# Optimization experiments

Hardware: AMD Instinct MI355X
Metric: run time of the kernel (lower is better)

The kernel has to match this reference:

```python
import jax, jax.numpy as jnp
import numpy as np

IMG = 512
LEVELS = (2, 3, 4, 5, 6)
SIZES = (16.0, 32.0, 64.0, 128.0, 256.0)
SCALES = tuple(2.0 ** (i / 3.0) for i in range(3))
ASPECTS = (0.5, 1.0, 2.0)
PRE_NMS = 1000
POST_NMS = 1000
IOU_T = 0.7
SCORE_T = 0.0
CROP = 7
NUM_CLASSES = 80

PARAMS = ('w_l2','b_l2','w_l3','b_l3','w_l4','b_l4','w_l5','b_l5','w_l6','b_l6',
          'w_o2','b_o2','w_o3','b_o3','w_o4','b_o4','w_o5','b_o5','w_o6','b_o6',
          'w_rpn','b_rpn','w_obj','b_obj','w_dlt','b_dlt',
          'w_fc1','b_fc1','w_fc2','b_fc2','w_box','b_box','w_cls','b_cls')

def conv(x, w, b, relu=False):
    y = jax.lax.conv_general_dilated(x, w, (1, 1), 'SAME', dimension_numbers=('NHWC', 'HWIO', 'NHWC')) + b
    return jax.nn.relu(y) if relu else y

def upsample2(x):
    return jnp.repeat(jnp.repeat(x, 2, axis=1), 2, axis=2)

def maxpool2(x):
    return jax.lax.reduce_window(x, -jnp.inf, jax.lax.max, (1, 2, 2, 1), (1, 2, 2, 1), 'VALID')

def make_anchors():
    # keras_cv AnchorGenerator: yxyx, 3 scales x 3 aspect ratios per location, clipped to image
    levels = []
    for lvl, size in zip(LEVELS, SIZES):
        stride = 2 ** lvl
        fs = IMG // stride
        ctr = (np.arange(fs) + 0.5) * stride
        hw = np.array([[size * sc / np.sqrt(ar), size * sc * np.sqrt(ar)] for sc in SCALES for ar in ASPECTS])
        cyx = np.stack(np.meshgrid(ctr, ctr, indexing='ij'), -1)  # [fs,fs,2]
        a = np.concatenate([cyx[:, :, None, :] - hw / 2.0, cyx[:, :, None, :] + hw / 2.0], -1).reshape(-1, 4)
        levels.append(np.clip(a, 0.0, IMG))
    return jnp.asarray(np.concatenate(levels, 0), jnp.float32)  # [196416,4]

def fpn(c2, c3, c4, c5, p):
    c6 = maxpool2(c5)
    p6 = conv(c6, p['w_l6'], p['b_l6'])
    p5 = conv(c5, p['w_l5'], p['b_l5']) + upsample2(p6)
    p4 = conv(c4, p['w_l4'], p['b_l4']) + upsample2(p5)
    p3 = conv(c3, p['w_l3'], p['b_l3']) + upsample2(p4)
    p2 = conv(c2, p['w_l2'], p['b_l2']) + upsample2(p3)
    return [conv(x, p['w_o%d' % l], p['b_o%d' % l]) for x, l in zip((p2, p3, p4, p5, p6), LEVELS)]

def rpn(fmaps, p):
    boxes, scores = [], []
    for f in fmaps:
        t = conv(f, p['w_rpn'], p['b_rpn'], relu=True)
        s = conv(t, p['w_obj'], p['b_obj'])
        d = conv(t, p['w_dlt'], p['b_dlt'])
        B = f.shape[0]
        boxes.append(d.reshape(B, -1, 4))
        scores.append(s.reshape(B, -1))
    return jnp.concatenate(boxes, 1), jnp.concatenate(scores, 1)

def decode(anchors, deltas):
    # _decode_deltas_to_boxes (no variance) then center_yxhw -> yxyx
    ahw = anchors[:, 2:] - anchors[:, :2]
    act = anchors[:, :2] + ahw * 0.5
    cyx = deltas[..., :2] * ahw + act
    hw = jnp.exp(deltas[..., 2:]) * ahw
    return jnp.concatenate([cyx - hw * 0.5, cyx + hw * 0.5], -1)

def nms_single(boxes, scores):
    # greedy NMS on top PRE_NMS proposals, padded to POST_NMS outputs
    sc, order = jax.lax.top_k(scores, PRE_NMS)
    b = boxes[order]
    y1, x1, y2, x2 = b[:, 0], b[:, 1], b[:, 2], b[:, 3]
    area = (y2 - y1) * (x2 - x1)

    def body(i, keep):
        iy1 = jnp.maximum(y1[i], y1)
        ix1 = jnp.maximum(x1[i], x1)
        iy2 = jnp.minimum(y2[i], y2)
        ix2 = jnp.minimum(x2[i], x2)
        inter = jnp.maximum(iy2 - iy1, 0.0) * jnp.maximum(ix2 - ix1, 0.0)
        iou = inter / (area[i] + area - inter + 1e-8)
        suppress = (iou > IOU_T) & (jnp.arange(PRE_NMS) > i) & keep[i]
        return keep & (~suppress)

    keep = jax.lax.fori_loop(0, PRE_NMS, body, sc > SCORE_T)
    idx = jnp.cumsum(keep) - 1
    slot = jnp.where(keep & (idx < POST_NMS), idx, POST_NMS)
    return jnp.zeros((POST_NMS, 4), boxes.dtype).at[slot].set(b, mode='drop')

def pad_stack(fmaps):
    Hm = fmaps[0].shape[1]
    return jnp.stack([jnp.pad(f, ((0, 0), (0, Hm - f.shape[1]), (0, Hm - f.shape[2]), (0, 0))) for f in fmaps], 1)

def roi_align(feats, rois):
    # multilevel crop-and-resize: 14x14 bilinear samples (offset 0.5) -> 2x2 avg pool -> 7x7
    S = CROP * 2

    def one(feat, box):
        h = box[2] - box[0]
        w = box[3] - box[1]
        size = jnp.sqrt(jnp.maximum(h * w, 1e-8))
        lvl = jnp.clip(jnp.floor(jnp.log2(size / 224.0) + 4.0), 2, 6).astype(jnp.int32)
        stride_i = jnp.left_shift(1, lvl)
        stride = stride_i.astype(jnp.float32)
        fs_i = IMG // stride_i
        fs = fs_i.astype(jnp.float32)
        yy = jnp.clip(box[0] / stride + (jnp.arange(S) + 0.5) * (h / stride) / S - 0.5, 0.0, fs - 1.0)
        xx = jnp.clip(box[1] / stride + (jnp.arange(S) + 0.5) * (w / stride) / S - 0.5, 0.0, fs - 1.0)
        y0 = jnp.floor(yy).astype(jnp.int32)
        x0 = jnp.floor(xx).astype(jnp.int32)
        y1 = jnp.minimum(y0 + 1, fs_i - 1)
        x1 = jnp.minimum(x0 + 1, fs_i - 1)
        wy = (yy - y0)[:, None, None]
        wx = (xx - x0)[None, :, None]
        fm = feat[lvl - 2]
        v00 = fm[y0[:, None], x0[None, :]]
        v01 = fm[y0[:, None], x1[None, :]]
        v10 = fm[y1[:, None], x0[None, :]]
        v11 = fm[y1[:, None], x1[None, :]]
        val = (1.0 - wy) * ((1.0 - wx) * v00 + wx * v01) + wy * ((1.0 - wx) * v10 + wx * v11)
        return val.reshape(CROP, 2, CROP, 2, val.shape[-1]).mean(axis=(1, 3))

    return jax.vmap(lambda f, r: jax.vmap(lambda b: one(f, b))(r))(feats, rois)

def forward(c2, c3, c4, c5, p):
    fmaps = fpn(c2, c3, c4, c5, p)
    rpn_boxes, rpn_scores = rpn(fmaps, p)
    anchors = make_anchors()
    decoded = decode(anchors, rpn_boxes)
    rois = jax.lax.stop_gradient(jax.vmap(nms_single)(decoded, rpn_scores))  # [B,1000,4]
    feats = roi_align(pad_stack(fmaps), rois)  # [B,1000,7,7,256]
    B, R = feats.shape[0], feats.shape[1]
    x = feats.reshape(B, R, -1)
    x = jax.nn.relu(x @ p['w_fc1'] + p['b_fc1'])
    x = jax.nn.relu(x @ p['w_fc2'] + p['b_fc2'])
    return rois, x @ p['w_box'] + p['b_box'], x @ p['w_cls'] + p['b_cls']

def setup_inputs() -> dict:
    key = jax.random.key(0)
    ks = iter(jax.random.split(key, 64))
    def rnd(shape, s=1.0):
        return jax.random.normal(next(ks), shape, jnp.float32) * s
    B = 2
    inp = {
        'c2': rnd((B, 128, 128, 256)), 'c3': rnd((B, 64, 64, 512)),
        'c4': rnd((B, 32, 32, 1024)), 'c5': rnd((B, 16, 16, 2048)),
    }
    lat_in = {2: 256, 3: 512, 4: 1024, 5: 2048, 6: 2048}
    for l in LEVELS:
        inp['w_l%d' % l] = rnd((1, 1, lat_in[l], 256), 0.02)
        inp['b_l%d' % l] = jnp.zeros((256,), jnp.float32)
        inp['w_o%d' % l] = rnd((3, 3, 256, 256), 0.02)
        inp['b_o%d' % l] = jnp.zeros((256,), jnp.float32)
    inp['w_rpn'] = rnd((3, 3, 256, 256), 0.02); inp['b_rpn'] = jnp.zeros((256,), jnp.float32)
    inp['w_obj'] = rnd((1, 1, 256, 9), 0.02); inp['b_obj'] = jnp.zeros((9,), jnp.float32)
    inp['w_dlt'] = rnd((1, 1, 256, 36), 0.02); inp['b_dlt'] = jnp.zeros((36,), jnp.float32)
    F = CROP * CROP * 256
    inp['w_fc1'] = rnd((F, 1024), 0.01); inp['b_fc1'] = jnp.zeros((1024,), jnp.float32)
    inp['w_fc2'] = rnd((1024, 1024), 0.02); inp['b_fc2'] = jnp.zeros((1024,), jnp.float32)
    inp['w_box'] = rnd((1024, 4), 0.02); inp['b_box'] = jnp.zeros((4,), jnp.float32)
    inp['w_cls'] = rnd((1024, NUM_CLASSES + 1), 0.02); inp['b_cls'] = jnp.zeros((NUM_CLASSES + 1,), jnp.float32)
    return inp

def reference(c2, c3, c4, c5, w_l2, b_l2, w_l3, b_l3, w_l4, b_l4, w_l5, b_l5, w_l6, b_l6,
              w_o2, b_o2, w_o3, b_o3, w_o4, b_o4, w_o5, b_o5, w_o6, b_o6,
              w_rpn, b_rpn, w_obj, b_obj, w_dlt, b_dlt,
              w_fc1, b_fc1, w_fc2, b_fc2, w_box, b_box, w_cls, b_cls):
    loc = locals()
    p = {k: loc[k] for k in PARAMS}
    return forward(c2, c3, c4, c5, p)
```

## Files before the change

### kernel.cpp

```cpp
#include <hip/hip_runtime.h>
#include <math.h>


#define NUM_ANCH 196416

typedef double d4 __attribute__((ext_vector_type(4)));
typedef __attribute__((ext_vector_type(8))) short bf8_t;
typedef __attribute__((ext_vector_type(4))) float f4_t;
typedef _Float16 h8_t __attribute__((ext_vector_type(8)));

__device__ inline unsigned short f2bf(float x) {
  unsigned u = __float_as_uint(x);
  unsigned r = (u + 0x7fffu + ((u >> 16) & 1u)) >> 16;
  return (unsigned short)r;
}
__device__ inline float bf2f(unsigned short h) {
  return __uint_as_float(((unsigned)h) << 16);
}

__global__ void maxpool_kernel(const float* __restrict__ in, float* __restrict__ out) {
  int idx = blockIdx.x * 256 + threadIdx.x;
  int c = idx & 2047;
  int x = (idx >> 11) & 7;
  int y = (idx >> 14) & 7;
  int b = idx >> 17;
  const float* p = in + (((size_t)b * 16 + 2 * y) * 16 + 2 * x) * 2048 + c;
  float m = fmaxf(fmaxf(p[0], p[2048]), fmaxf(p[16 * 2048], p[16 * 2048 + 2048]));
  out[idx] = m;
}

template <int CIN>
__global__ __launch_bounds__(256) void lateral_d(
    const float* __restrict__ in, const float* __restrict__ w,
    const float* __restrict__ bias, double* __restrict__ out) {
  const int t = threadIdx.x;
  const size_t pix0 = (size_t)blockIdx.x * 4;
  double b = (double)bias[t];
  double a0 = b, a1 = b, a2 = b, a3 = b;
  const float* i0 = in + pix0 * CIN;
  for (int ci = 0; ci < CIN; ++ci) {
    double wv = (double)w[ci * 256 + t];
    a0 += (double)i0[ci] * wv;
    a1 += (double)i0[CIN + ci] * wv;
    a2 += (double)i0[2 * CIN + ci] * wv;
    a3 += (double)i0[3 * CIN + ci] * wv;
  }
  out[(pix0 + 0) * 256 + t] = a0;
  out[(pix0 + 1) * 256 + t] = a1;
  out[(pix0 + 2) * 256 + t] = a2;
  out[(pix0 + 3) * 256 + t] = a3;
}

__global__ void upadd_d(double* __restrict__ fine, const double* __restrict__ coarse,
                        int Hf, int Wf) {
  int idx = blockIdx.x * 256 + threadIdx.x;
  int c = idx & 255;
  int rem = idx >> 8;
  int x = rem % Wf; rem /= Wf;
  int y = rem % Hf;
  int b = rem / Hf;
  fine[idx] += coarse[(((size_t)b * (Hf >> 1) + (y >> 1)) * (Wf >> 1) + (x >> 1)) * 256 + c];
}

__global__ __launch_bounds__(256) void wsplit_f16(
    const float* __restrict__ W, unsigned short* __restrict__ PH,
    unsigned short* __restrict__ PL) {
  int id = blockIdx.x * 256 + threadIdx.x;
  int co = id & 255, ci = (id >> 8) & 255, p9 = id >> 16;
  float w = W[id];
  _Float16 wh = (_Float16)w;
  float rw = (w - (float)wh) * 4096.0f;
  _Float16 wl = (_Float16)rw;
  int q = (p9 * 8 + (ci >> 5)) * 16 + (co >> 4);
  int idx = q * 512 + (co & 15) * 32 + (ci & 31);
  PH[idx] = __builtin_bit_cast(unsigned short, wh);
  PL[idx] = __builtin_bit_cast(unsigned short, wl);
}

struct ConvArgsU {
  const double* inD[5];
  const unsigned short* inH[5];
  const unsigned short* inL[5];
  float* outF[5];
  unsigned short* outH[5];
  unsigned short* outL[5];
  double* outD[5];
  const unsigned short* wH[5];
  const unsigned short* wL[5];
  const float* bias[5];
  int H[5];
  int nbx[5];
  int off[6];
};

template <bool PLANES, bool RELU, bool OSPLIT>
__global__ __launch_bounds__(512, 4) void conv3x3_u(ConvArgsU A) {
  __shared__ uint4 smemq[34816 / 16];
  char* sh = (char*)smemq;
  const int bx = blockIdx.x;
  int l = 0;
#pragma unroll
  for (int i = 1; i < 5; ++i)
    if (bx >= A.off[i]) l = i;
  const int rel = bx - A.off[l];
  const int H = A.H[l];
  const int W = H;
  const int nbx = A.nbx[l];
  const int x0 = (rel % nbx) * 32;
  const int y = (rel / nbx) % H;
  const int b = rel / (nbx * H);
  const unsigned short* __restrict__ wHp = A.wH[l];
  const unsigned short* __restrict__ wLp = A.wL[l];
  const float* __restrict__ bias = A.bias[l];

  const int t = threadIdx.x;
  const int lane = t & 63;
  const int wq = t >> 6;
  const int lm = lane & 15;
  const int lq = lane >> 4;

  d4 dacc[2][2];
#pragma unroll
  for (int mt = 0; mt < 2; ++mt)
#pragma unroll
    for (int nt = 0; nt < 2; ++nt) {
      double bv = (double)bias[wq * 32 + nt * 16 + lm];
      dacc[mt][nt] = (d4){bv, bv, bv, bv};
    }

  const int cst = (t & 127) * 2;
  const int prow = t >> 7;
  const int c16 = (t & 31) * 8;
  const int pp0 = t >> 5;

  for (int ky = 0; ky < 3; ++ky) {
    const int gy = y + ky - 1;
    const bool rowok = (gy >= 0 && gy < H);
    __syncthreads();
    if (PLANES) {
      const unsigned short* __restrict__ inH = A.inH[l];
      const unsigned short* __restrict__ inL = A.inL[l];
      for (int pp = pp0; pp < 34; pp += 16) {
        int gx = x0 + pp - 1;
        uint4 vh = {0u, 0u, 0u, 0u}, vl = {0u, 0u, 0u, 0u};
        if (rowok && gx >= 0 && gx < W) {
          size_t base = (((size_t)b * H + gy) * W + gx) * 256 + c16;
          vh = *(const uint4*)&inH[base];
          vl = *(const uint4*)&inL[base];
        }
        int bo = pp * 512 + ((c16 * 2) ^ ((pp & 7) << 4));
        *(uint4*)(sh + bo) = vh;
        *(uint4*)(sh + 17408 + bo) = vl;
      }
    } else {
      const double* __restrict__ inD = A.inD[l];
      for (int pp = prow; pp < 34; pp += 4) {
        int gx = x0 + pp - 1;
        double xv0 = 0.0, xv1 = 0.0;
        if (rowok && gx >= 0 && gx < W) {
          const double* ptr = inD + (((size_t)b * H + gy) * W + gx) * 256 + cst;
          xv0 = ptr[0];
          xv1 = ptr[1];
        }
        _Float16 h0 = (_Float16)((float)xv0);
        _Float16 h1 = (_Float16)((float)xv1);
        float r0 = (float)(xv0 - (double)(float)h0) * 4096.0f;
        float r1 = (float)(xv1 - (double)(float)h1) * 4096.0f;
        _Float16 l0 = (_Float16)r0, l1 = (_Float16)r1;
        unsigned hp = (unsigned)__builtin_bit_cast(unsigned short, h0) |
                      ((unsigned)__builtin_bit_cast(unsigned short, h1) << 16);
        unsigned lp = (unsigned)__builtin_bit_cast(unsigned short, l0) |
                      ((unsigned)__builtin_bit_cast(unsigned short, l1) << 16);
        int bo = pp * 512 + ((cst * 2) ^ ((pp & 7) << 4));
        *(unsigned*)(sh + bo) = hp;
        *(unsigned*)(sh + 17408 + bo) = lp;
      }
    }
    __syncthreads();

    f4_t accA[2][2], accB[2][2];
#pragma unroll
    for (int mt = 0; mt < 2; ++mt)
#pragma unroll
      for (int nt = 0; nt < 2; ++nt) {
        accA[mt][nt] = (f4_t){0.f, 0.f, 0.f, 0.f};
        accB[mt][nt] = (f4_t){0.f, 0.f, 0.f, 0.f};
      }

    for (int kx = 0; kx < 3; ++kx) {
      const int P0 = (ky * 3 + kx) * 8;
      for (int kt = 0; kt < 8; ++kt) {
        h8_t aH[2], aL[2];
#pragma unroll
        for (int mt = 0; mt < 2; ++mt) {
          int pix = mt * 16 + lm + kx;
          int bo = pix * 512 + ((kt * 64 + lq * 16) ^ ((pix & 7) << 4));
          aH[mt] = *(const h8_t*)(sh + bo);
          aL[mt] = *(const h8_t*)(sh + 17408 + bo);
        }
#pragma unroll
        for (int nt = 0; nt < 2; ++nt) {
          size_t eo = (size_t)((P0 + kt) * 16 + wq * 2 + nt) * 512 + lm * 32 + lq * 8;
          h8_t bH = *(const h8_t*)(wHp + eo);
          h8_t bL = *(const h8_t*)(wLp + eo);
#pragma unroll
          for (int mt = 0; mt < 2; ++mt) {
            accB[mt][nt] = __builtin_amdgcn_mfma_f32_16x16x32_f16(aH[mt], bL, accB[mt][nt], 0, 0, 0);
            accB[mt][nt] = __builtin_amdgcn_mfma_f32_16x16x32_f16(aL[mt], bH, accB[mt][nt], 0, 0, 0);
            accA[mt][nt] = __builtin_amdgcn_mfma_f32_16x16x32_f16(aH[mt], bH, accA[mt][nt], 0, 0, 0);
          }
        }
      }
    }
#pragma unroll
    for (int mt = 0; mt < 2; ++mt)
#pragma unroll
      for (int nt = 0; nt < 2; ++nt)
#pragma unroll
        for (int r = 0; r < 4; ++r)
          dacc[mt][nt][r] += (double)accA[mt][nt][r] +
                             (double)accB[mt][nt][r] * (1.0 / 4096.0);
  }

#pragma unroll
  for (int mt = 0; mt < 2; ++mt)
#pragma unroll
    for (int nt = 0; nt < 2; ++nt) {
      int cout = wq * 32 + nt * 16 + lm;
#pragma unroll
      for (int r = 0; r < 4; ++r) {
        int gx = x0 + mt * 16 + lq * 4 + r;
        if (gx < W) {
          double v = dacc[mt][nt][r];
          if (RELU) v = fmax(v, 0.0);
          size_t idx = (((size_t)b * H + y) * W + gx) * 256 + cout;
          if (OSPLIT) {
            _Float16 hh = (_Float16)((float)v);
            float rr = (float)(v - (double)(float)hh) * 4096.0f;
            _Float16 ll = (_Float16)rr;
            A.outF[l][idx] = (float)v;
            A.outH[l][idx] = __builtin_bit_cast(unsigned short, hh);
            A.outL[l][idx] = __builtin_bit_cast(unsigned short, ll);
          } else {
            A.outD[l][idx] = v;
          }
        }
      }
    }
}

struct AnchorHW { double hh[9]; double ww[9]; };

__global__ __launch_bounds__(64) void rpn_head_d(
    const double* __restrict__ tmap,
    const float* __restrict__ w_obj, const float* __restrict__ b_obj,
    const float* __restrict__ w_dlt, const float* __restrict__ b_dlt,
    double* __restrict__ scores, double* __restrict__ boxes,
    int H, int W, int a_off, double stride, AnchorHW anc) {
  __shared__ double tv[256];
  __shared__ double dlt[36];
  const int t = threadIdx.x;
  const int x = blockIdx.x, y = blockIdx.y, b = blockIdx.z;
  const double* px = tmap + (((size_t)b * H + y) * W + x) * 256;
  tv[t] = px[t]; tv[t + 64] = px[t + 64]; tv[t + 128] = px[t + 128]; tv[t + 192] = px[t + 192];
  __syncthreads();
  double sacc = 0.0;
  if (t < 9) {
    sacc = (double)b_obj[t];
    for (int ci = 0; ci < 256; ++ci) sacc += tv[ci] * (double)w_obj[ci * 9 + t];
  } else if (t < 45) {
    int j = t - 9;
    double a = (double)b_dlt[j];
    for (int ci = 0; ci < 256; ++ci) a += tv[ci] * (double)w_dlt[ci * 36 + j];
    dlt[j] = a;
  }
  __syncthreads();
  if (t < 9) {
    int ai = a_off + (y * W + x) * 9 + t;
    scores[(size_t)b * NUM_ANCH + ai] = sacc;
    double cy = (y + 0.5) * stride, cx = (x + 0.5) * stride;
    double hh = anc.hh[t], ww = anc.ww[t];
    float ay1 = (float)fmin(fmax(cy - hh * 0.5, 0.0), 512.0);
    float ax1 = (float)fmin(fmax(cx - ww * 0.5, 0.0), 512.0);
    float ay2 = (float)fmin(fmax(cy + hh * 0.5, 0.0), 512.0);
    float ax2 = (float)fmin(fmax(cx + ww * 0.5, 0.0), 512.0);
    float ahf = ay2 - ay1, awf = ax2 - ax1;
    float actyf = ay1 + ahf * 0.5f, actxf = ax1 + awf * 0.5f;
    double dy = dlt[t * 4 + 0], dx = dlt[t * 4 + 1];
    double dh = dlt[t * 4 + 2], dw = dlt[t * 4 + 3];
    double ncy = dy * (double)ahf + (double)actyf;
    double ncx = dx * (double)awf + (double)actxf;
    double nh = exp(dh) * (double)ahf;
    double nw = exp(dw) * (double)awf;
    double* bo = boxes + ((size_t)b * NUM_ANCH + ai) * 4;
    bo[0] = ncy - nh * 0.5;
    bo[1] = ncx - nw * 0.5;
    bo[2] = ncy + nh * 0.5;
    bo[3] = ncx + nw * 0.5;
  }
}

__device__ inline unsigned long long dkey(double f) {
  unsigned long long u = (unsigned long long)__double_as_longlong(f);
  return u ^ ((unsigned long long)((long long)u >> 63) | 0x8000000000000000ull);
}

__global__ __launch_bounds__(1024) void topk_d(
    const double* __restrict__ scores, const double* __restrict__ boxes,
    double* __restrict__ ss, double* __restrict__ sb) {
  const int A = NUM_ANCH;
  __shared__ unsigned hist[256];
  __shared__ unsigned long long kk[2048];
  __shared__ unsigned id[2048];
  __shared__ unsigned long long s_prefix;
  __shared__ unsigned s_need, s_cnt;
  const int b = blockIdx.x, t = threadIdx.x;
  const double* sc = scores + (size_t)b * A;
  if (t == 0) { s_prefix = 0ull; s_need = 1000; s_cnt = 0; }
  __syncthreads();
  for (int r = 0; r < 8; ++r) {
    if (t < 256) hist[t] = 0;
    __syncthreads();
    const int shift = 56 - 8 * r;
    const unsigned long long prefix = s_prefix;
    unsigned long long maskHigh = 0ull;
    if (r != 0) maskHigh = (~0ull) << (shift + 8);
    for (int i = t; i < A; i += 1024) {
      unsigned long long k = dkey(sc[i]);
      if ((k & maskHigh) == prefix) atomicAdd(&hist[(unsigned)(k >> shift) & 255u], 1u);
    }
    __syncthreads();
    if (t == 0) {
      unsigned need = s_need, cum = 0;
      for (int bin = 255; bin >= 0; --bin) {
        cum += hist[bin];
        if (cum >= need) {
          s_prefix = prefix | ((unsigned long long)bin << shift);
          s_need = need - (cum - hist[bin]);
          break;
        }
      }
    }
    __syncthreads();
  }
  const unsigned long long K = s_prefix;
  for (int i = t; i < A; i += 1024) {
    unsigned long long k = dkey(sc[i]);
    if (k >= K) {
      unsigned pos = atomicAdd(&s_cnt, 1u);
      if (pos < 2048) { kk[pos] = k; id[pos] = (unsigned)i; }
    }
  }
  __syncthreads();
  unsigned cnt = s_cnt;
  for (int i = t; i < 2048; i += 1024)
    if (i >= cnt) { kk[i] = 0ull; id[i] = 0xFFFFFFFFu; }
  __syncthreads();
  for (int k = 2; k <= 2048; k <<= 1) {
    for (int j = k >> 1; j > 0; j >>= 1) {
#pragma unroll
      for (int u = 0; u < 2; ++u) {
        int i = t + u * 1024;
        int ixj = i ^ j;
        if (ixj > i) {
          unsigned long long ka = kk[i], kc = kk[ixj];
          unsigned ia = id[i], ic = id[ixj];
          bool cPrec = (kc > ka) || (kc == ka && ic < ia);
          bool up = (i & k) != 0;
          if (cPrec != up) { kk[i] = kc; kk[ixj] = ka; id[i] = ic; id[ixj] = ia; }
        }
      }
      __syncthreads();
    }
  }
  if (t < 1000) {
    unsigned idx = id[t];
    ss[b * 1000 + t] = sc[idx];
    const double* bp = boxes + ((size_t)b * A + idx) * 4;
    double* op = sb + (b * 1000 + t) * 4;
    op[0] = bp[0]; op[1] = bp[1]; op[2] = bp[2]; op[3] = bp[3];
  }
}

__global__ void suppmat_d(const double* __restrict__ sb,
                          unsigned long long* __restrict__ supp) {
  int g = blockIdx.x * 256 + threadIdx.x;
  int w = g & 15;
  int i = (g >> 4) % 1000;
  int b = g / 16000;
  const double* bx = sb + b * 4000;
  double y1 = bx[i * 4 + 0], x1 = bx[i * 4 + 1], y2 = bx[i * 4 + 2], x2 = bx[i * 4 + 3];
  double ai = (y2 - y1) * (x2 - x1);
  unsigned long long m = 0;
  for (int q = 0; q < 64; ++q) {
    int j = w * 64 + q;
    if (j > i && j < 1000) {
      double by1 = bx[j * 4 + 0], bx1 = bx[j * 4 + 1], by2 = bx[j * 4 + 2], bx2 = bx[j * 4 + 3];
      double aj = (by2 - by1) * (bx2 - bx1);
      double iy1 = fmax(y1, by1), ix1 = fmax(x1, bx1);
      double iy2 = fmin(y2, by2), ix2 = fmin(x2, bx2);
      double inter = fmax(iy2 - iy1, 0.0) * fmax(ix2 - ix1, 0.0);
      double iou = inter / (ai + aj - inter + 1e-8);
      if (iou > 0.7) m |= (1ull << q);
    }
  }
  supp[g] = m;
}

__global__ __launch_bounds__(64) void nms_reduce_d(
    const double* __restrict__ ss, const double* __restrict__ sb,
    const unsigned long long* __restrict__ supp,
    float* __restrict__ rois, double* __restrict__ rois64) {
  __shared__ unsigned long long aliveS[16];
  __shared__ int pref[16];
  const int b = blockIdx.x, lane = threadIdx.x;
  unsigned long long myword = 0;
  if (lane < 16) {
    for (int q = 0; q < 64; ++q) {
      int j = lane * 64 + q;
      if (j < 1000 && ss[b * 1000 + j] > 0.0) myword |= (1ull << q);
    }
  }
  const unsigned long long* sp = supp + (size_t)b * 16000;
  unsigned long long cur = (lane < 16) ? sp[lane] : 0ull;
  for (int i = 0; i < 1000; ++i) {
    unsigned long long nxt = (lane < 16 && i < 999) ? sp[(i + 1) * 16 + lane] : 0ull;
    unsigned long long wv = __shfl(myword, i >> 6);
    if ((wv >> (i & 63)) & 1ull) {
      if (lane < 16) myword &= ~cur;
    }
    cur = nxt;
  }
  if (lane < 16) aliveS[lane] = myword;
  __syncthreads();
  if (lane == 0) {
    int s = 0;
    for (int w = 0; w < 16; ++w) { pref[w] = s; s += __popcll(aliveS[w]); }
  }
  float* ro = rois + b * 4000;
  double* rd = rois64 + b * 4000;
  for (int k = lane; k < 4000; k += 64) { ro[k] = 0.0f; rd[k] = 0.0; }
  __syncthreads();
  for (int j = lane; j < 1000; j += 64) {
    int w = j >> 6;
    unsigned long long word = aliveS[w];
    if ((word >> (j & 63)) & 1ull) {
      unsigned long long below = (j & 63) ? (word & ((1ull << (j & 63)) - 1ull)) : 0ull;
      int slot = pref[w] + __popcll(below);
      const double* bp = sb + (b * 1000 + j) * 4;
      ro[slot * 4 + 0] = (float)bp[0]; ro[slot * 4 + 1] = (float)bp[1];
      ro[slot * 4 + 2] = (float)bp[2]; ro[slot * 4 + 3] = (float)bp[3];
      rd[slot * 4 + 0] = bp[0]; rd[slot * 4 + 1] = bp[1];
      rd[slot * 4 + 2] = bp[2]; rd[slot * 4 + 3] = bp[3];
    }
  }
}

__global__ __launch_bounds__(256) void roi_align_d(
    const float* __restrict__ o2, const float* __restrict__ o3,
    const float* __restrict__ o4, const float* __restrict__ o5,
    const float* __restrict__ o6, const double* __restrict__ rois64,
    unsigned short* __restrict__ featsH, unsigned short* __restrict__ featsL) {
  __shared__ double s_wy[14], s_wx[14];
  __shared__ int s_y0[14], s_y1[14], s_x0[14], s_x1[14];
  const int t = threadIdx.x;
  const int b = blockIdx.x / 1000, r = blockIdx.x % 1000;
  const double* box = rois64 + (b * 1000 + r) * 4;
  double b0 = box[0], b1 = box[1], b2 = box[2], b3 = box[3];
  double h = b2 - b0, w = b3 - b1;
  double size = sqrt(fmax(h * w, 1e-8));
  double lf = floor(log2(size / 224.0) + 4.0);
  lf = fmin(fmax(lf, 2.0), 6.0);
  int lvl = (int)lf;
  int stride_i = 1 << lvl;
  double stride = (double)stride_i;
  int fs_i = 512 >> lvl;
  double fs = (double)fs_i;
  if (t < 14) {
    double v = b0 / stride + ((t + 0.5) * (h / stride)) / 14.0 - 0.5;
    v = fmin(fmax(v, 0.0), fs - 1.0);
    int i0 = (int)floor(v);
    s_y0[t] = i0; s_y1[t] = min(i0 + 1, fs_i - 1); s_wy[t] = v - (double)i0;
  } else if (t >= 64 && t < 78) {
    int u = t - 64;
    double v = b1 / stride + ((u + 0.5) * (w / stride)) / 14.0 - 0.5;
    v = fmin(fmax(v, 0.0), fs - 1.0);
    int i0 = (int)floor(v);
    s_x0[u] = i0; s_x1[u] = min(i0 + 1, fs_i - 1); s_wx[u] = v - (double)i0;
  }
  __syncthreads();
  const float* omaps[5] = {o2, o3, o4, o5, o6};
  const float* fm = omaps[lvl - 2] + (size_t)b * fs_i * fs_i * 256 + t;
  size_t obase = ((size_t)(b * 1000 + r) * 49) * 256 + t;
  for (int oy = 0; oy < 7; ++oy) {
    double acc[7] = {0, 0, 0, 0, 0, 0, 0};
#pragma unroll
    for (int sy = 0; sy < 2; ++sy) {
      int yy = oy * 2 + sy;
      int y0 = s_y0[yy], y1 = s_y1[yy];
      double wy = s_wy[yy];
      const float* r0 = fm + (size_t)y0 * fs_i * 256;
      const float* r1 = fm + (size_t)y1 * fs_i * 256;
      for (int ox = 0; ox < 7; ++ox) {
#pragma unroll
        for (int sx = 0; sx < 2; ++sx) {
          int xx = ox * 2 + sx;
          int x0 = s_x0[xx], x1 = s_x1[xx];
          double wx = s_wx[xx];
          double v00 = (double)r0[x0 * 256], v01 = (double)r0[x1 * 256];
          double v10 = (double)r1[x0 * 256], v11 = (double)r1[x1 * 256];
          double val = (1.0 - wy) * ((1.0 - wx) * v00 + wx * v01) +
                       wy * ((1.0 - wx) * v10 + wx * v11);
          acc[ox] += val;
        }
      }
    }
    for (int ox = 0; ox < 7; ++ox) {
      float v = (float)(acc[ox] * 0.25);
      unsigned short hh = f2bf(v);
      size_t idx = obase + (size_t)(oy * 7 + ox) * 256;
      featsH[idx] = hh;
      featsL[idx] = f2bf(v - bf2f(hh));
    }
  }
}

__global__ __launch_bounds__(256) void split_transpose(
    const float* __restrict__ W, unsigned short* __restrict__ TH,
    unsigned short* __restrict__ TL, int K, int N) {
  __shared__ unsigned short shh[32 * 33], shl[32 * 33];
  const int kt = blockIdx.y * 32, nt = blockIdx.x * 32;
  const int tx = threadIdx.x & 31, ty = threadIdx.x >> 5;
  for (int yy = ty; yy < 32; yy += 8) {
    float v = W[(size_t)(kt + yy) * N + nt + tx];
    unsigned short h = f2bf(v);
    shh[yy * 33 + tx] = h;
    shl[yy * 33 + tx] = f2bf(v - bf2f(h));
  }
  __syncthreads();
  for (int yy = ty; yy < 32; yy += 8) {
    TH[(size_t)(nt + yy) * K + kt + tx] = shh[tx * 33 + yy];
    TL[(size_t)(nt + yy) * K + kt + tx] = shl[tx * 33 + yy];
  }
}

struct GemmPArgs {
  const unsigned short* AH;
  const unsigned short* AL;
  const unsigned short* BTH;
  const unsigned short* BTL;
  float* P[4];
  int M, N, K, KC;
};

__global__ __launch_bounds__(256) void gemm_mfma_partial(GemmPArgs G) {
  __shared__ __align__(16) unsigned short AsH[128 * 40], AsL[128 * 40];
  __shared__ __align__(16) unsigned short BsH[128 * 40], BsL[128 * 40];
  const int t = threadIdx.x;
  const int lane = t & 63;
  const int wave = t >> 6;
  const int lm = lane & 15, lq = lane >> 4;
  const int wn = wave & 1, wm = wave >> 1;
  const int m0 = blockIdx.y * 128, n0 = blockIdx.x * 128;
  const int kc = blockIdx.z;
  const int kbeg = kc * G.KC, kend = kbeg + G.KC;
  const int M = G.M, N = G.N, K = G.K;
  float* __restrict__ C = G.P[kc];
  const unsigned short* __restrict__ AH = G.AH;
  const unsigned short* __restrict__ AL = G.AL;
  const unsigned short* __restrict__ BTH = G.BTH;
  const unsigned short* __restrict__ BTL = G.BTL;
  const int sr = t >> 1;
  const int sk = (t & 1) * 16;

  f4_t acc[4][4];
#pragma unroll
  for (int mt = 0; mt < 4; ++mt)
#pragma unroll
    for (int nt = 0; nt < 4; ++nt) acc[mt][nt] = (f4_t){0.f, 0.f, 0.f, 0.f};

  const uint4 zz = {0u, 0u, 0u, 0u};
  for (int k0 = kbeg; k0 < kend; k0 += 32) {
    __syncthreads();
    {
      uint4 vh0 = zz, vh1 = zz, vl0 = zz, vl1 = zz;
      if (m0 + sr < M) {
        size_t off = (size_t)(m0 + sr) * K + k0 + sk;
        vh0 = *(const uint4*)&AH[off];
        vh1 = *(const uint4*)&AH[off + 8];
        vl0 = *(const uint4*)&AL[off];
        vl1 = *(const uint4*)&AL[off + 8];
      }
      *(uint4*)&AsH[sr * 40 + sk] = vh0;
      *(uint4*)&AsH[sr * 40 + sk + 8] = vh1;
      *(uint4*)&AsL[sr * 40 + sk] = vl0;
      *(uint4*)&AsL[sr * 40 + sk + 8] = vl1;
    }
    {
      size_t off = (size_t)(n0 + sr) * K + k0 + sk;
      *(uint4*)&BsH[sr * 40 + sk] = *(const uint4*)&BTH[off];
      *(uint4*)&BsH[sr * 40 + sk + 8] = *(const uint4*)&BTH[off + 8];
      *(uint4*)&BsL[sr * 40 + sk] = *(const uint4*)&BTL[off];
      *(uint4*)&BsL[sr * 40 + sk + 8] = *(const uint4*)&BTL[off + 8];
    }
    __syncthreads();

    bf8_t aH[4], aL[4], bH[4], bL[4];
#pragma unroll
    for (int mt = 0; mt < 4; ++mt) {
      int idx = (wm * 64 + mt * 16 + lm) * 40 + lq * 8;
      aH[mt] = *(const bf8_t*)&AsH[idx];
      aL[mt] = *(const bf8_t*)&AsL[idx];
    }
#pragma unroll
    for (int nt = 0; nt < 4; ++nt) {
      int idx = (wn * 64 + nt * 16 + lm) * 40 + lq * 8;
      bH[nt] = *(const bf8_t*)&BsH[idx];
      bL[nt] = *(const bf8_t*)&BsL[idx];
    }
#pragma unroll
    for (int mt = 0; mt < 4; ++mt)
#pragma unroll
      for (int nt = 0; nt < 4; ++nt) {
        f4_t a0 = acc[mt][nt];
        a0 = __builtin_amdgcn_mfma_f32_16x16x32_bf16(aL[mt], bH[nt], a0, 0, 0, 0);
        a0 = __builtin_amdgcn_mfma_f32_16x16x32_bf16(aH[mt], bL[nt], a0, 0, 0, 0);
        a0 = __builtin_amdgcn_mfma_f32_16x16x32_bf16(aH[mt], bH[nt], a0, 0, 0, 0);
        acc[mt][nt] = a0;
      }
  }
#pragma unroll
  for (int mt = 0; mt < 4; ++mt) {
#pragma unroll
    for (int nt = 0; nt < 4; ++nt) {
      int ncol = n0 + wn * 64 + nt * 16 + lm;
#pragma unroll
      for (int r = 0; r < 4; ++r) {
        int m = m0 + wm * 64 + mt * 16 + lq * 4 + r;
        if (m < M) C[(size_t)m * N + ncol] = acc[mt][nt][r];
      }
    }
  }
}

__global__ void reduce4_split(const float* __restrict__ p0, const float* __restrict__ p1,
                              const float* __restrict__ p2, const float* __restrict__ p3,
                              const float* __restrict__ bias,
                              unsigned short* __restrict__ H, unsigned short* __restrict__ L,
                              int n) {
  int i = blockIdx.x * 256 + threadIdx.x;
  if (i < n) {
    float v = ((p0[i] + p1[i]) + p2[i]) + p3[i] + bias[i & 1023];
    v = fmaxf(v, 0.0f);
    unsigned short h = f2bf(v);
    H[i] = h;
    L[i] = f2bf(v - bf2f(h));
  }
}

__global__ void reduce4_f32(const float* __restrict__ p0, const float* __restrict__ p1,
                            const float* __restrict__ p2, const float* __restrict__ p3,
                            const float* __restrict__ bias, float* __restrict__ C, int n) {
  int i = blockIdx.x * 256 + threadIdx.x;
  if (i < n) {
    float v = ((p0[i] + p1[i]) + p2[i]) + p3[i] + bias[i & 1023];
    C[i] = fmaxf(v, 0.0f);
  }
}

__global__ __launch_bounds__(128) void boxcls_kernel(
    const float* __restrict__ x, const float* __restrict__ w_box,
    const float* __restrict__ b_box, const float* __restrict__ w_cls,
    const float* __restrict__ b_cls, float* __restrict__ out) {
  __shared__ float xv[1024];
  const int t = threadIdx.x;
  const int row = blockIdx.x;
  const float* xp = x + (size_t)row * 1024;
#pragma unroll
  for (int k = 0; k < 8; ++k) xv[k * 128 + t] = xp[k * 128 + t];
  __syncthreads();
  if (t < 4) {
    float acc = b_box[t];
    for (int k = 0; k < 1024; ++k) acc += xv[k] * w_box[k * 4 + t];
    out[8000 + row * 4 + t] = acc;
  } else if (t < 85) {
    int j = t - 4;
    float acc = b_cls[j];
    for (int k = 0; k < 1024; ++k) acc += xv[k] * w_cls[k * 81 + j];
    out[16000 + row * 81 + j] = acc;
  }
}

extern "C" void kernel_launch(void* const* d_in, const int* in_sizes, int n_in,
                              void* d_out, int out_size, void* d_ws, size_t ws_size,
                              hipStream_t stream) {
  (void)in_sizes; (void)n_in; (void)out_size; (void)ws_size;

  const float* c_in[4] = {(const float*)d_in[0], (const float*)d_in[1],
                          (const float*)d_in[2], (const float*)d_in[3]};
  const float *w_l[5], *b_l[5], *w_o[5], *b_o[5];
  for (int l = 0; l < 5; ++l) {
    w_l[l] = (const float*)d_in[4 + l * 4 + 0];
    b_l[l] = (const float*)d_in[4 + l * 4 + 1];
    w_o[l] = (const float*)d_in[4 + l * 4 + 2];
    b_o[l] = (const float*)d_in[4 + l * 4 + 3];
  }
  const float* w_rpn = (const float*)d_in[24];
  const float* b_rpn = (const float*)d_in[25];
  const float* w_obj = (const float*)d_in[26];
  const float* b_obj = (const float*)d_in[27];
  const float* w_dlt = (const float*)d_in[28];
  const float* b_dlt = (const float*)d_in[29];
  const float* w_fc1 = (const float*)d_in[30];
  const float* b_fc1 = (const float*)d_in[31];
  const float* w_fc2 = (const float*)d_in[32];
  const float* b_fc2 = (const float*)d_in[33];
  const float* w_box = (const float*)d_in[34];
  const float* b_box = (const float*)d_in[35];
  const float* w_cls = (const float*)d_in[36];
  const float* b_cls = (const float*)d_in[37];

  char* W8 = (char*)d_ws;
  float* oF32 = (float*)(W8 + 0);
  unsigned short* oH = (unsigned short*)(W8 + 44695552);
  unsigned short* oL = (unsigned short*)(W8 + 67043328);
  double* p64 = (double*)(W8 + 89391104);
  float* c6buf = (float*)(W8 + 178782208);
  double* scores = (double*)(W8 + 179830784);
  double* boxes = (double*)(W8 + 182973440);
  double* ssb = (double*)(W8 + 195544064);
  double* sbb = (double*)(W8 + 195560064);
  double* rois64 = (double*)(W8 + 195624064);
  unsigned long long* suppb = (unsigned long long*)(W8 + 195688064);
  unsigned short* featsH = (unsigned short*)(W8 + 89391104);
  unsigned short* featsL = (unsigned short*)(W8 + 139567104);
  float* fc1b = (float*)(W8 + 0);
  float* fc2b = (float*)(W8 + 8192000);
  unsigned short* wT1H = (unsigned short*)(W8 + 16384000);
  unsigned short* wT1L = (unsigned short*)(W8 + 42074112);
  unsigned short* wT2H = (unsigned short*)(W8 + 67764224);
  unsigned short* wT2L = (unsigned short*)(W8 + 69861376);
  unsigned short* fc1H = (unsigned short*)(W8 + 89391104);
  unsigned short* fc1L = (unsigned short*)(W8 + 93487104);
  float* fc1p1 = (float*)(W8 + 8192000);
  float* fc1p2 = (float*)(W8 + 71958528);
  float* fc1p3 = (float*)(W8 + 80150528);
  float* fc2p1 = (float*)(W8 + 0);
  float* fc2p2 = (float*)(W8 + 16384000);
  float* fc2p3 = (float*)(W8 + 24576000);
  float* outf = (float*)d_out;

  unsigned short* woH[5];
  unsigned short* woL[5];
  for (int l = 0; l < 5; ++l) {
    woH[l] = (unsigned short*)(W8 + 182973440 + (size_t)l * 2359296);
    woL[l] = (unsigned short*)(W8 + 182973440 + (size_t)l * 2359296 + 1179648);
  }
  unsigned short* wrH = (unsigned short*)(W8 + 179830784);
  unsigned short* wrL = (unsigned short*)(W8 + 179830784 + 1179648);

  const size_t OFF[5] = {0, 8388608, 10485760, 11010048, 11141120};
  const int HS[5] = {128, 64, 32, 16, 8};
  const int a_off[5] = {0, 147456, 184320, 193536, 195840};
  const double strides[5] = {4.0, 8.0, 16.0, 32.0, 64.0};
  const double SZ[5] = {16.0, 32.0, 64.0, 128.0, 256.0};
  AnchorHW anc[5];
  for (int l = 0; l < 5; ++l) {
    const double ars[3] = {0.5, 1.0, 2.0};
    for (int s = 0; s < 3; ++s) {
      double sc = pow(2.0, s / 3.0);
      for (int a = 0; a < 3; ++a) {
        double sq = sqrt(ars[a]);
        anc[l].hh[s * 3 + a] = SZ[l] * sc / sq;
        anc[l].ww[s * 3 + a] = SZ[l] * sc * sq;
      }
    }
  }

  for (int l = 0; l < 5; ++l)
    wsplit_f16<<<2304, 256, 0, stream>>>(w_o[l], woH[l], woL[l]);
  wsplit_f16<<<2304, 256, 0, stream>>>(w_rpn, wrH, wrL);

  maxpool_kernel<<<1024, 256, 0, stream>>>(c_in[3], c6buf);
  lateral_d<2048><<<32, 256, 0, stream>>>(c6buf, w_l[4], b_l[4], p64 + OFF[4]);
  lateral_d<2048><<<128, 256, 0, stream>>>(c_in[3], w_l[3], b_l[3], p64 + OFF[3]);
  upadd_d<<<512, 256, 0, stream>>>(p64 + OFF[3], p64 + OFF[4], 16, 16);
  lateral_d<1024><<<512, 256, 0, stream>>>(c_in[2], w_l[2], b_l[2], p64 + OFF[2]);
  upadd_d<<<2048, 256, 0, stream>>>(p64 + OFF[2], p64 + OFF[3], 32, 32);
  lateral_d<512><<<2048, 256, 0, stream>>>(c_in[1], w_l[1], b_l[1], p64 + OFF[1]);
  upadd_d<<<8192, 256, 0, stream>>>(p64 + OFF[1], p64 + OFF[2], 64, 64);
  lateral_d<256><<<8192, 256, 0, stream>>>(c_in[0], w_l[0], b_l[0], p64 + OFF[0]);
  upadd_d<<<32768, 256, 0, stream>>>(p64 + OFF[0], p64 + OFF[1], 128, 128);

  ConvArgsU co, ct;
  int total = 0;
  for (int l = 0; l < 5; ++l) {
    int nbx = (HS[l] + 31) / 32;
    co.inD[l] = p64 + OFF[l]; co.inH[l] = nullptr; co.inL[l] = nullptr;
    co.outF[l] = oF32 + OFF[l]; co.outH[l] = oH + OFF[l]; co.outL[l] = oL + OFF[l];
    co.outD[l] = nullptr;
    co.wH[l] = woH[l]; co.wL[l] = woL[l]; co.bias[l] = b_o[l];
    ct.inD[l] = nullptr; ct.inH[l] = oH + OFF[l]; ct.inL[l] = oL + OFF[l];
    ct.outF[l] = nullptr; ct.outH[l] = nullptr; ct.outL[l] = nullptr;
    ct.outD[l] = p64 + OFF[l];
    ct.wH[l] = wrH;  ct.wL[l] = wrL;  ct.bias[l] = b_rpn;
    co.H[l] = ct.H[l] = HS[l];
    co.nbx[l] = ct.nbx[l] = nbx;
    co.off[l] = ct.off[l] = total;
    total += nbx * HS[l] * 2;
  }
  co.off[5] = ct.off[5] = total;
  conv3x3_u<false, false, true><<<total, 512, 0, stream>>>(co);
  conv3x3_u<true, true, false><<<total, 512, 0, stream>>>(ct);

  for (int l = 0; l < 5; ++l) {
    dim3 g(HS[l], HS[l], 2);
    rpn_head_d<<<g, 64, 0, stream>>>(p64 + OFF[l], w_obj, b_obj, w_dlt, b_dlt,
                                     scores, boxes, HS[l], HS[l], a_off[l],
                                     strides[l], anc[l]);
  }
  topk_d<<<2, 1024, 0, stream>>>(scores, boxes, ssb, sbb);
  suppmat_d<<<125, 256, 0, stream>>>(sbb, suppb);
  nms_reduce_d<<<2, 64, 0, stream>>>(ssb, sbb, suppb, outf, rois64);
  roi_align_d<<<2000, 256, 0, stream>>>(oF32 + OFF[0], oF32 + OFF[1], oF32 + OFF[2],
                                        oF32 + OFF[3], oF32 + OFF[4], rois64,
                                        featsH, featsL);
  split_transpose<<<dim3(32, 392), 256, 0, stream>>>(w_fc1, wT1H, wT1L, 12544, 1024);
  split_transpose<<<dim3(32, 32), 256, 0, stream>>>(w_fc2, wT2H, wT2L, 1024, 1024);

  GemmPArgs g1;
  g1.AH = featsH; g1.AL = featsL; g1.BTH = wT1H; g1.BTL = wT1L;
  g1.P[0] = fc1b; g1.P[1] = fc1p1; g1.P[2] = fc1p2; g1.P[3] = fc1p3;
  g1.M = 2000; g1.N = 1024; g1.K = 12544; g1.KC = 3136;
  gemm_mfma_partial<<<dim3(8, 16, 4), 256, 0, stream>>>(g1);
  reduce4_split<<<8000, 256, 0, stream>>>(fc1b, fc1p1, fc1p2, fc1p3, b_fc1,
                                          fc1H, fc1L, 2048000);

  GemmPArgs g2;
  g2.AH = fc1H; g2.AL = fc1L; g2.BTH = wT2H; g2.BTL = wT2L;
  g2.P[0] = fc2b; g2.P[1] = fc2p1; g2.P[2] = fc2p2; g2.P[3] = fc2p3;
  g2.M = 2000; g2.N = 1024; g2.K = 1024; g2.KC = 256;
  gemm_mfma_partial<<<dim3(8, 16, 4), 256, 0, stream>>>(g2);
  reduce4_f32<<<8000, 256, 0, stream>>>(fc2b, fc2p1, fc2p2, fc2p3, b_fc2,
                                        fc2b, 2048000);

  boxcls_kernel<<<2000, 128, 0, stream>>>(fc2b, w_box, b_box, w_cls, b_cls, outf);
}
```

Baseline: 3.096 ms.

## Split top-k radix select into multi-block histogram, pick, collect, and sort kernels

Replaces the single two-block top-k kernel with a multi-kernel pipeline. Global histograms are built across 64 blocks per image, using three 11-bit radix passes instead of eight 8-bit ones. A separate kernel picks the threshold bin each pass, candidates are collected into global buffers, and a final kernel bitonic-sorts them. This spreads the memory-bound score scans over many CUs, at the cost of extra launches and a coarser threshold that may admit more candidates, risking overflow of the 2048-entry buffer.

```diff
diff --git a/kernel.cpp b/kernel.cpp
--- a/kernel.cpp
+++ b/kernel.cpp
@@ -305,56 +305,100 @@
   return u ^ ((unsigned long long)((long long)u >> 63) | 0x8000000000000000ull);
 }
 
-__global__ __launch_bounds__(1024) void topk_d(
+__global__ void topk_init(unsigned* __restrict__ hist,
+                          unsigned long long* __restrict__ prefix,
+                          unsigned* __restrict__ need, unsigned* __restrict__ cnt) {
+  int t = blockIdx.x * 256 + threadIdx.x;
+  if (t < 2 * 3 * 2048) hist[t] = 0;
+  if (t < 2) { prefix[t] = 0ull; need[t] = 1000; cnt[t] = 0; }
+}
+
+__global__ __launch_bounds__(256) void topk_hist(
+    const double* __restrict__ scores, const unsigned long long* __restrict__ prefix,
+    unsigned* __restrict__ hist, int shift, unsigned long long maskHigh) {
+  const int b = blockIdx.y;
+  __shared__ unsigned lh[2048];
+  for (int i = threadIdx.x; i < 2048; i += 256) lh[i] = 0;
+  __syncthreads();
+  const double* sc = scores + (size_t)b * NUM_ANCH;
+  const unsigned long long pfx = prefix[b];
+  const int stride = gridDim.x * 256;
+  for (int i = blockIdx.x * 256 + threadIdx.x; i < NUM_ANCH; i += stride) {
+    unsigned long long k = dkey(sc[i]);
+    if ((k & maskHigh) == pfx)
+      atomicAdd(&lh[(unsigned)(k >> shift) & 2047u], 1u);
+  }
+  __syncthreads();
+  unsigned* gh = hist + b * 2048;
+  for (int i = threadIdx.x; i < 2048; i += 256) {
+    unsigned v = lh[i];
+    if (v) atomicAdd(&gh[i], v);
+  }
+}
+
+__global__ __launch_bounds__(1024) void topk_pick(
+    const unsigned* __restrict__ hist, unsigned long long* __restrict__ prefix,
+    unsigned* __restrict__ need, int shift) {
+  const int b = blockIdx.x;
+  __shared__ unsigned s[2048];
+  const unsigned* gh = hist + b * 2048;
+  const int t = threadIdx.x;
+  s[t] = gh[t];
+  s[t + 1024] = gh[t + 1024];
+  __syncthreads();
+  for (int off = 1; off < 2048; off <<= 1) {
+    unsigned v0 = s[t] + ((t + off < 2048) ? s[t + off] : 0u);
+    unsigned v1 = s[t + 1024] + ((t + 1024 + off < 2048) ? s[t + 1024 + off] : 0u);
+    __syncthreads();
+    s[t] = v0;
+    s[t + 1024] = v1;
+    __syncthreads();
+  }
+  const unsigned nd = need[b];
+#pragma unroll
+  for (int u = 0; u < 2; ++u) {
+    int bin = t + u * 1024;
+    unsigned Sb = s[bin];
+    unsigned Sa = (bin < 2047) ? s[bin + 1] : 0u;
+    if (Sb >= nd && Sa < nd) {
+      prefix[b] |= ((unsigned long long)bin) << shift;
+      need[b] = nd - Sa;
+    }
+  }
+}
+
+__global__ __launch_bounds__(256) void topk_collect(
+    const double* __restrict__ scores, const unsigned long long* __restrict__ prefix,
+    unsigned* __restrict__ cnt, unsigned long long* __restrict__ ckey,
+    unsigned* __restrict__ cid) {
+  const int b = blockIdx.y;
+  const double* sc = scores + (size_t)b * NUM_ANCH;
+  const unsigned long long K = prefix[b];
+  const int stride = gridDim.x * 256;
+  for (int i = blockIdx.x * 256 + threadIdx.x; i < NUM_ANCH; i += stride) {
+    unsigned long long k = dkey(sc[i]);
+    if (k >= K) {
+      unsigned pos = atomicAdd(&cnt[b], 1u);
+      if (pos < 2048) { ckey[b * 2048 + pos] = k; cid[b * 2048 + pos] = (unsigned)i; }
+    }
+  }
+}
+
+__global__ __launch_bounds__(1024) void topk_final(
     const double* __restrict__ scores, const double* __restrict__ boxes,
-    double* __restrict__ ss, double* __restrict__ sb) {
-  const int A = NUM_ANCH;
-  __shared__ unsigned hist[256];
+    const unsigned* __restrict__ cnt, const unsigned long long* __restrict__ ckey,
+    const unsigned* __restrict__ cid, double* __restrict__ ss,
+    double* __restrict__ sb) {
+  const int b = blockIdx.x;
   __shared__ unsigned long long kk[2048];
   __shared__ unsigned id[2048];
-  __shared__ unsigned long long s_prefix;
-  __shared__ unsigned s_need, s_cnt;
-  const int b = blockIdx.x, t = threadIdx.x;
-  const double* sc = scores + (size_t)b * A;
-  if (t == 0) { s_prefix = 0ull; s_need = 1000; s_cnt = 0; }
-  __syncthreads();
-  for (int r = 0; r < 8; ++r) {
-    if (t < 256) hist[t] = 0;
-    __syncthreads();
-    const int shift = 56 - 8 * r;
-    const unsigned long long prefix = s_prefix;
-    unsigned long long maskHigh = 0ull;
-    if (r != 0) maskHigh = (~0ull) << (shift + 8);
-    for (int i = t; i < A; i += 1024) {
-      unsigned long long k = dkey(sc[i]);
-      if ((k & maskHigh) == prefix) atomicAdd(&hist[(unsigned)(k >> shift) & 255u], 1u);
-    }
-    __syncthreads();
-    if (t == 0) {
-      unsigned need = s_need, cum = 0;
-      for (int bin = 255; bin >= 0; --bin) {
-        cum += hist[bin];
-        if (cum >= need) {
-          s_prefix = prefix | ((unsigned long long)bin << shift);
-          s_need = need - (cum - hist[bin]);
-          break;
-        }
-      }
-    }
-    __syncthreads();
-  }
-  const unsigned long long K = s_prefix;
-  for (int i = t; i < A; i += 1024) {
-    unsigned long long k = dkey(sc[i]);
-    if (k >= K) {
-      unsigned pos = atomicAdd(&s_cnt, 1u);
-      if (pos < 2048) { kk[pos] = k; id[pos] = (unsigned)i; }
-    }
-  }
-  __syncthreads();
-  unsigned cnt = s_cnt;
-  for (int i = t; i < 2048; i += 1024)
-    if (i >= cnt) { kk[i] = 0ull; id[i] = 0xFFFFFFFFu; }
+  const int t = threadIdx.x;
+  unsigned c = cnt[b];
+  if (c > 2048u) c = 2048u;
+  for (int i = t; i < 2048; i += 1024) {
+    if (i < (int)c) { kk[i] = ckey[b * 2048 + i]; id[i] = cid[b * 2048 + i]; }
+    else { kk[i] = 0ull; id[i] = 0xFFFFFFFFu; }
+  }
   __syncthreads();
   for (int k = 2; k <= 2048; k <<= 1) {
     for (int j = k >> 1; j > 0; j >>= 1) {
@@ -375,8 +419,8 @@
   }
   if (t < 1000) {
     unsigned idx = id[t];
-    ss[b * 1000 + t] = sc[idx];
-    const double* bp = boxes + ((size_t)b * A + idx) * 4;
+    ss[b * 1000 + t] = scores[(size_t)b * NUM_ANCH + idx];
+    const double* bp = boxes + ((size_t)b * NUM_ANCH + idx) * 4;
     double* op = sb + (b * 1000 + t) * 4;
     op[0] = bp[0]; op[1] = bp[1]; op[2] = bp[2]; op[3] = bp[3];
   }
@@ -750,6 +794,13 @@
   float* fc2p3 = (float*)(W8 + 24576000);
   float* outf = (float*)d_out;
 
+  unsigned* tk_hist = (unsigned*)(W8 + 44695552);
+  unsigned long long* tk_prefix = (unsigned long long*)(W8 + 44744704);
+  unsigned* tk_need = (unsigned*)(W8 + 44744720);
+  unsigned* tk_cnt = (unsigned*)(W8 + 44744728);
+  unsigned long long* tk_ckey = (unsigned long long*)(W8 + 44744768);
+  unsigned* tk_cid = (unsigned*)(W8 + 44777536);
+
   unsigned short* woH[5];
   unsigned short* woL[5];
   for (int l = 0; l < 5; ++l) {
@@ -819,7 +870,22 @@
                                      scores, boxes, HS[l], HS[l], a_off[l],
                                      strides[l], anc[l]);
   }
-  topk_d<<<2, 1024, 0, stream>>>(scores, boxes, ssb, sbb);
+
+  topk_init<<<48, 256, 0, stream>>>(tk_hist, tk_prefix, tk_need, tk_cnt);
+  const int tk_shift[3] = {53, 42, 31};
+  for (int lv = 0; lv < 3; ++lv) {
+    unsigned long long maskHigh = lv ? ((~0ull) << (tk_shift[lv] + 11)) : 0ull;
+    topk_hist<<<dim3(64, 2), 256, 0, stream>>>(scores, tk_prefix,
+                                               tk_hist + lv * 4096,
+                                               tk_shift[lv], maskHigh);
+    topk_pick<<<2, 1024, 0, stream>>>(tk_hist + lv * 4096, tk_prefix, tk_need,
+                                      tk_shift[lv]);
+  }
+  topk_collect<<<dim3(64, 2), 256, 0, stream>>>(scores, tk_prefix, tk_cnt,
+                                                tk_ckey, tk_cid);
+  topk_final<<<2, 1024, 0, stream>>>(scores, boxes, tk_cnt, tk_ckey, tk_cid,
+                                     ssb, sbb);
+
   suppmat_d<<<125, 256, 0, stream>>>(sbb, suppb);
   nms_reduce_d<<<2, 64, 0, stream>>>(ssb, sbb, suppb, outf, rois64);
   roi_align_d<<<2000, 256, 0, stream>>>(oF32 + OFF[0], oF32 + OFF[1], oF32 + OFF[2],
```

Result: faster. 2.763 ms (-10.7%).
